# Kernel optimization log

Hardware: AMD Instinct MI355X
Metric: run time of the kernel (lower is better)

The kernel has to match this reference:

```python
import jax, jax.numpy as jnp
import numpy as np
from jax import lax

SCORE_THRESH = 0.05
NMS_THRESH = 0.5
DETECTIONS_PER_IMG = 100
MIN_SIZE = 0.01
AREA_THRESH = 0.0
BOX_W = (10.0, 10.0, 5.0, 5.0)
BBOX_XFORM_CLIP = float(np.log(1000.0 / 16.0))


def setup_inputs() -> dict:
    key = jax.random.key(0)
    B, N, C = 8, 4000, 91
    H, W = 800, 1333
    k1, k2, k3 = jax.random.split(key, 3)
    # scale logits so a realistic fraction of softmax scores exceed score_thresh
    class_logits = jax.random.normal(k1, (B * N, C), jnp.float32) * 2.0
    box_regression = jax.random.normal(k2, (B * N, C * 4), jnp.float32)
    u = jax.random.uniform(k3, (B, N, 4), jnp.float32)
    x1 = u[..., 0] * (W - 50)
    y1 = u[..., 1] * (H - 50)
    bw = u[..., 2] * 200.0 + 4.0
    bh = u[..., 3] * 200.0 + 4.0
    proposals = jnp.stack([x1, y1, jnp.minimum(x1 + bw, W), jnp.minimum(y1 + bh, H)], axis=-1)
    return {"class_logits": class_logits, "box_regression": box_regression,
            "proposals": proposals, "image_h": H, "image_w": W}


def _decode(rel, props):
    # torchvision BoxCoder.decode: props [P,4], rel [P, C*4] -> [P, C, 4]
    w = props[:, 2] - props[:, 0]
    h = props[:, 3] - props[:, 1]
    cx = props[:, 0] + 0.5 * w
    cy = props[:, 1] + 0.5 * h
    rel = rel.reshape(rel.shape[0], -1, 4)
    dx = rel[..., 0] / BOX_W[0]
    dy = rel[..., 1] / BOX_W[1]
    dw = jnp.minimum(rel[..., 2] / BOX_W[2], BBOX_XFORM_CLIP)
    dh = jnp.minimum(rel[..., 3] / BOX_W[3], BBOX_XFORM_CLIP)
    pcx = dx * w[:, None] + cx[:, None]
    pcy = dy * h[:, None] + cy[:, None]
    pw = jnp.exp(dw) * w[:, None]
    ph = jnp.exp(dh) * h[:, None]
    return jnp.stack([pcx - 0.5 * pw, pcy - 0.5 * ph, pcx + 0.5 * pw, pcy + 0.5 * ph], axis=-1)


def _nms_image(boxes, scores, labels_f, valid, off_unit):
    # greedy batched NMS (class-offset trick) producing first DETECTIONS_PER_IMG survivors
    NEG = -1e9
    s0 = jnp.where(valid, scores, NEG)
    ob = boxes + (labels_f * off_unit)[:, None]  # per-class coordinate offset
    areas = (ob[:, 2] - ob[:, 0]) * (ob[:, 3] - ob[:, 1])

    def step(s, _):
        i = jnp.argmax(s)
        sc = s[i]
        ok = sc > (NEG / 2)
        obi = ob[i]
        ix1 = jnp.maximum(obi[0], ob[:, 0])
        iy1 = jnp.maximum(obi[1], ob[:, 1])
        ix2 = jnp.minimum(obi[2], ob[:, 2])
        iy2 = jnp.minimum(obi[3], ob[:, 3])
        inter = jnp.maximum(ix2 - ix1, 0.0) * jnp.maximum(iy2 - iy1, 0.0)
        ai = (obi[2] - obi[0]) * (obi[3] - obi[1])
        iou = inter / jnp.maximum(ai + areas - inter, 1e-9)
        sup = (iou > NMS_THRESH) & ok
        s = jnp.where(sup, NEG, s).at[i].set(NEG)
        return s, (i, jnp.where(ok, sc, 0.0), ok)

    _, (idx, out_sc, ok) = lax.scan(step, s0, None, length=DETECTIONS_PER_IMG)
    out_boxes = boxes[idx] * ok[:, None]
    out_labels = jnp.where(ok, labels_f[idx], 0.0)
    areas_out = (out_boxes[:, 2] - out_boxes[:, 0]) * (out_boxes[:, 3] - out_boxes[:, 1])
    keep = ok & (areas_out >= AREA_THRESH)
    return out_boxes * keep[:, None], out_sc * keep, jnp.where(keep, out_labels, 0.0), keep


def reference(class_logits, box_regression, proposals, image_h, image_w):
    B, N, _ = proposals.shape
    C = class_logits.shape[-1]
    pred_boxes = _decode(box_regression, proposals.reshape(B * N, 4)).reshape(B, N, C, 4)
    pred_scores = jax.nn.softmax(class_logits, axis=-1).reshape(B, N, C)
    # clip boxes to image
    x = jnp.clip(pred_boxes[..., 0::2], 0.0, float(image_w))
    y = jnp.clip(pred_boxes[..., 1::2], 0.0, float(image_h))
    pred_boxes = jnp.stack([x[..., 0], y[..., 0], x[..., 1], y[..., 1]], axis=-1)
    # drop background class 0, flatten (proposal, class) pairs
    M = N * (C - 1)
    boxes = pred_boxes[:, :, 1:, :].reshape(B, M, 4)
    scores = pred_scores[:, :, 1:].reshape(B, M)
    labels_f = jnp.broadcast_to(jnp.arange(1, C, dtype=boxes.dtype)[None, :], (N, C - 1)).reshape(M)
    ws = boxes[..., 2] - boxes[..., 0]
    hs = boxes[..., 3] - boxes[..., 1]
    valid = (scores > SCORE_THRESH) & (ws >= MIN_SIZE) & (hs >= MIN_SIZE)
    off_unit = float(max(image_h, image_w)) + 1.0
    out_boxes, out_scores, out_labels_f, keep = jax.vmap(
        lambda b, s, v: _nms_image(b, s, labels_f, v, off_unit))(boxes, scores, valid)
    return out_boxes, out_scores, out_labels_f.astype(jnp.int32), keep
```

## Files before the change

### kernel.cpp

```cpp
#include <hip/hip_runtime.h>
#include <stdint.h>

typedef uint32_t u32;
typedef unsigned long long u64;

#define NB 8
#define NPER 4000
#define NC 91
#define NCLS 90
#define NDET 100
#define CHUNKS 64
#define RPB 63
#define LBIN 16
#define CCAP 63
#define BINCAP 512
#define SURVCAP 9216
#define NSFIX (NCLS * NDET)
#define FKCAP 1024
#define VPT 36

__device__ __forceinline__ float4 decode_clip(float4 rel, float w, float h,
                                              float cx, float cy, float W, float H) {
  const float XCLIP = 4.135166556742356f;
  float dx = rel.x / 10.0f;
  float dy = rel.y / 10.0f;
  float dw = fminf(rel.z / 5.0f, XCLIP);
  float dh = fminf(rel.w / 5.0f, XCLIP);
  float qcx = dx * w + cx;
  float qcy = dy * h + cy;
  float qw = expf(dw) * w;
  float qh = expf(dh) * h;
  float x1 = qcx - 0.5f * qw, y1 = qcy - 0.5f * qh;
  float x2 = qcx + 0.5f * qw, y2 = qcy + 0.5f * qh;
  x1 = fminf(fmaxf(x1, 0.0f), W);
  x2 = fminf(fmaxf(x2, 0.0f), W);
  y1 = fminf(fmaxf(y1, 0.0f), H);
  y2 = fminf(fmaxf(y2, 0.0f), H);
  return make_float4(x1, y1, x2, y2);
}

__device__ __forceinline__ float rdlane(float v, int sl) {
  return __int_as_float(__builtin_amdgcn_readlane(__float_as_int(v), sl));
}

__device__ __forceinline__ void emit_row(int r, int rl, int lane, float sA, float sB,
    float W, float H, const float4* __restrict__ props4, const float4* __restrict__ breg4,
    u32* s_cnt, u64 (*s_key)[LBIN], float4 (*s_box)[LBIN],
    size_t chbase, u64* __restrict__ bins_key, float4* __restrict__ bins_box) {
  bool eA_ok = (lane >= 1) && (sA > 0.05f);
  bool eB_ok = (lane < NC - 64) && (sB > 0.05f);
  if (!(eA_ok || eB_ok)) return;
  float4 p = props4[r];
  float w = p.z - p.x, h = p.w - p.y;
  float cx = p.x + 0.5f * w, cy = p.y + 0.5f * h;
  if (eA_ok) {
    float4 raw = decode_clip(breg4[(size_t)r * NC + lane], w, h, cx, cy, W, H);
    if (((raw.z - raw.x) >= 0.01f) && ((raw.w - raw.y) >= 0.01f)) {
      int ci = lane - 1;
      u32 orig = (u32)(rl * NCLS + ci);
      u64 key = ((u64)__float_as_uint(sA) << 22) | (u64)(0x3FFFFFu - orig);
      u32 lp = atomicAdd(&s_cnt[ci], 1u);
      if (lp < LBIN) { s_key[ci][lp] = key; s_box[ci][lp] = raw; }
      else if (lp < CCAP) {
        size_t o = (chbase + ci) * CCAP + lp;
        bins_key[o] = key; bins_box[o] = raw;
      }
    }
  }
  if (eB_ok) {
    float4 raw = decode_clip(breg4[(size_t)r * NC + 64 + lane], w, h, cx, cy, W, H);
    if (((raw.z - raw.x) >= 0.01f) && ((raw.w - raw.y) >= 0.01f)) {
      int ci = 63 + lane;
      u32 orig = (u32)(rl * NCLS + ci);
      u64 key = ((u64)__float_as_uint(sB) << 22) | (u64)(0x3FFFFFu - orig);
      u32 lp = atomicAdd(&s_cnt[ci], 1u);
      if (lp < LBIN) { s_key[ci][lp] = key; s_box[ci][lp] = raw; }
      else if (lp < CCAP) {
        size_t o = (chbase + ci) * CCAP + lp;
        bins_key[o] = key; bins_box[o] = raw;
      }
    }
  }
}

__global__ __launch_bounds__(1024) void k_score(const float* __restrict__ logits,
    const float* __restrict__ boxreg, const float* __restrict__ props,
    const int* __restrict__ dh, const int* __restrict__ dw,
    u32* cnt_g, u64* bins_key, float4* bins_box) {
  __shared__ u64 s_key[NCLS][LBIN];
  __shared__ float4 s_box[NCLS][LBIN];
  __shared__ u32 s_cnt[NCLS];
  int tid = threadIdx.x;
  int b = blockIdx.x / CHUNKS;
  int chunk = blockIdx.x % CHUNKS;
  int wave = tid >> 6, lane = tid & 63;
  if (tid < NCLS) s_cnt[tid] = 0u;
  __syncthreads();

  float H = (float)dh[0], W = (float)dw[0];
  const float4* props4 = (const float4*)props;
  const float4* breg4 = (const float4*)boxreg;
  size_t chbase = ((size_t)(b * CHUNKS + chunk)) * NCLS;

  for (int rloc = wave; rloc < RPB; rloc += 32) {
    int rloc1 = rloc + 16;
    int rl0 = chunk * RPB + rloc;
    int rl1 = chunk * RPB + rloc1;
    bool v0 = (rl0 < NPER);
    bool v1 = (rloc1 < RPB) && (rl1 < NPER);
    int r0 = b * NPER + (v0 ? rl0 : 0);
    int r1 = b * NPER + (v1 ? rl1 : 0);
    const float* l0 = logits + (size_t)r0 * NC;
    const float* l1 = logits + (size_t)r1 * NC;
    float xA0 = l0[lane];
    float xA1 = l1[lane];
    float xB0 = (lane < NC - 64) ? l0[64 + lane] : -3.0e38f;
    float xB1 = (lane < NC - 64) ? l1[64 + lane] : -3.0e38f;
    float mx0 = fmaxf(xA0, xB0);
    float mx1 = fmaxf(xA1, xB1);
    for (int o = 32; o; o >>= 1) {
      mx0 = fmaxf(mx0, __shfl_xor(mx0, o));
      mx1 = fmaxf(mx1, __shfl_xor(mx1, o));
    }
    float eA0 = expf(xA0 - mx0);
    float eA1 = expf(xA1 - mx1);
    float eB0 = (lane < NC - 64) ? expf(xB0 - mx0) : 0.0f;
    float eB1 = (lane < NC - 64) ? expf(xB1 - mx1) : 0.0f;
    float sm0 = eA0 + eB0;
    float sm1 = eA1 + eB1;
    for (int o = 32; o; o >>= 1) {
      sm0 += __shfl_xor(sm0, o);
      sm1 += __shfl_xor(sm1, o);
    }
    if (v0) emit_row(r0, rl0, lane, eA0 / sm0, eB0 / sm0, W, H, props4, breg4,
                     s_cnt, s_key, s_box, chbase, bins_key, bins_box);
    if (v1) emit_row(r1, rl1, lane, eA1 / sm1, eB1 / sm1, W, H, props4, breg4,
                     s_cnt, s_key, s_box, chbase, bins_key, bins_box);
  }
  __syncthreads();
  if (tid < NCLS) cnt_g[chbase + tid] = s_cnt[tid];
  for (int idx = tid; idx < NCLS * LBIN; idx += 1024) {
    int ci = idx / LBIN, j = idx % LBIN;
    if ((u32)j < s_cnt[ci]) {
      size_t o = (chbase + ci) * CCAP + (u32)j;
      bins_key[o] = s_key[ci][j];
      bins_box[o] = s_box[ci][j];
    }
  }
}

__global__ __launch_bounds__(256) void k_nms_class(const u32* __restrict__ cnt_g,
    const u64* __restrict__ bins_key, const float4* __restrict__ bins_box,
    u64* skey, float4* sbox, const int* __restrict__ dh, const int* __restrict__ dw) {
  __shared__ u64 k[BINCAP];
  __shared__ float4 boxu[BINCAP];
  __shared__ u64 ks[BINCAP];
  __shared__ float4 boxs[BINCAP];
  __shared__ float4 s_sb[NDET];
  __shared__ float s_sa[NDET];
  __shared__ u64 s_sk[NDET];
  __shared__ u32 s_sid[NDET];
  __shared__ u32 s_off[64];
  __shared__ u32 s_c[64];
  __shared__ u32 s_n;

  int b = blockIdx.x / NCLS;
  int ci = blockIdx.x % NCLS;
  int tid = threadIdx.x;
  u64* outk = skey + (size_t)b * SURVCAP + (size_t)ci * NDET;
  float4* outb = sbox + (size_t)b * SURVCAP + (size_t)ci * NDET;

  if (tid < 64) {
    u32 c = cnt_g[((size_t)(b * CHUNKS + tid)) * NCLS + ci];
    if (c > CCAP) c = CCAP;
    s_c[tid] = c;
    u32 inc = c;
    for (int o = 1; o < 64; o <<= 1) {
      u32 v = __shfl_up(inc, o);
      if (tid >= o) inc += v;
    }
    s_off[tid] = inc - c;
    if (tid == 63) s_n = (inc > BINCAP) ? BINCAP : inc;
  }
  __syncthreads();
  int n = (int)s_n;
  if (n <= 0) {
    for (int i = tid; i < NDET; i += 256) outk[i] = 0ull;
    return;
  }
  {
    int chunk = tid & 63, start = tid >> 6;
    u32 cc = s_c[chunk], of = s_off[chunk];
    size_t src = (((size_t)(b * CHUNKS + chunk)) * NCLS + ci) * CCAP;
    for (u32 i = (u32)start; i < cc; i += 4) {
      u32 d = of + i;
      if (d < (u32)BINCAP) { k[d] = bins_key[src + i]; boxu[d] = bins_box[src + i]; }
    }
  }
  __syncthreads();
  for (int i = tid; i < n; i += 256) {
    u64 ki = k[i];
    u32 rank = 0;
    int j = 0;
    for (; j + 4 <= n; j += 4) {
      rank += (k[j] > ki) ? 1u : 0u;
      rank += (k[j + 1] > ki) ? 1u : 0u;
      rank += (k[j + 2] > ki) ? 1u : 0u;
      rank += (k[j + 3] > ki) ? 1u : 0u;
    }
    for (; j < n; ++j) rank += (k[j] > ki) ? 1u : 0u;
    ks[rank] = ki;
    boxs[rank] = boxu[i];
  }
  __syncthreads();
  if (tid >= 64) return;

  float H = (float)dh[0], W = (float)dw[0];
  float loff = (fmaxf(H, W) + 1.0f) * (float)(ci + 1);
  int lane = tid;
  int S = 0;
  for (int base = 0; base < n && S < NDET; base += 64) {
    int i = base + lane;
    bool have = (i < n);
    u64 mykey = 0ull;
    float4 Bb = make_float4(0.f, 0.f, 0.f, 0.f);
    float aB = 0.f;
    if (have) {
      mykey = ks[i];
      float4 raw = boxs[i];
      Bb = make_float4(raw.x + loff, raw.y + loff, raw.z + loff, raw.w + loff);
      aB = (Bb.z - Bb.x) * (Bb.w - Bb.y);
    }
    bool alive = have;
    for (int s = 0; s < S; ++s) {
      float4 A = s_sb[s];
      float aA = s_sa[s];
      float ix1 = fmaxf(A.x, Bb.x), iy1 = fmaxf(A.y, Bb.y);
      float ix2 = fminf(A.z, Bb.z), iy2 = fminf(A.w, Bb.w);
      float inter = fmaxf(ix2 - ix1, 0.0f) * fmaxf(iy2 - iy1, 0.0f);
      float iou = inter / fmaxf(aA + aB - inter, 1e-9f);
      if (alive && iou > 0.5f) alive = false;
    }
    u64 mask = __ballot(alive);
    while (mask && S < NDET) {
      int j = __builtin_ctzll(mask);
      int js = __builtin_amdgcn_readfirstlane(j);
      float Ax = rdlane(Bb.x, js), Ay = rdlane(Bb.y, js);
      float Az = rdlane(Bb.z, js), Aw = rdlane(Bb.w, js);
      float aA = rdlane(aB, js);
      if (lane == js) {
        s_sb[S] = Bb; s_sa[S] = aB; s_sk[S] = mykey; s_sid[S] = (u32)i;
      }
      float ix1 = fmaxf(Ax, Bb.x), iy1 = fmaxf(Ay, Bb.y);
      float ix2 = fminf(Az, Bb.z), iy2 = fminf(Aw, Bb.w);
      float inter = fmaxf(ix2 - ix1, 0.0f) * fmaxf(iy2 - iy1, 0.0f);
      float iou = inter / fmaxf(aA + aB - inter, 1e-9f);
      if (alive && iou > 0.5f) alive = false;
      ++S;
      mask = __ballot(alive);
    }
  }
  for (int i2 = lane; i2 < NDET; i2 += 64) {
    if (i2 < S) {
      outk[i2] = s_sk[i2];
      outb[i2] = boxs[s_sid[i2]];
    } else {
      outk[i2] = 0ull;
    }
  }
}

__global__ __launch_bounds__(256) void k_top(const u64* __restrict__ skey,
    const float4* __restrict__ sbox, float* out) {
  __shared__ u32 ssc[SURVCAP];
  __shared__ u32 s_red[4];
  __shared__ u32 s_cnt[2];
  __shared__ u64 fk[FKCAP];
  __shared__ u32 fs[FKCAP];
  __shared__ u64 okey[NDET];
  __shared__ u32 osrc[NDET];

  int b = blockIdx.x;
  int tid = threadIdx.x;
  const u64* kb = skey + (size_t)b * SURVCAP;

  u32 sc[VPT];
#pragma unroll
  for (int v = 0; v < VPT; ++v) {
    u32 j = (u32)tid + (u32)v * 256u;
    u32 s = 0u;
    if (j < NSFIX) s = (u32)(kb[j] >> 22);
    sc[v] = s;
    ssc[j] = s;
  }
  if (tid == 0) { s_cnt[0] = 0; s_cnt[1] = 0; }
  __syncthreads();

  u32 lo = 0x3D4CCCCEu, hi = 0x3F800001u;
  while (lo < hi) {
    u32 mid = lo + ((hi - lo) >> 1);
    u32 c = 0;
#pragma unroll
    for (int v = 0; v < VPT; ++v) c += (sc[v] > mid) ? 1u : 0u;
    for (int o = 32; o; o >>= 1) c += __shfl_xor(c, o);
    if ((tid & 63) == 0) s_red[tid >> 6] = c;
    __syncthreads();
    u32 totc = s_red[0] + s_red[1] + s_red[2] + s_red[3];
    __syncthreads();
    if (totc < NDET) hi = mid; else lo = mid + 1;
  }
  u32 T = lo;
  __syncthreads();

  for (u32 j = tid; j < NSFIX; j += 256) {
    if (ssc[j] > T) {
      u32 p = atomicAdd(&s_cnt[0], 1u);
      if (p < FKCAP) { fk[p] = kb[j]; fs[p] = j; }
    }
  }
  __syncthreads();
  if (tid == 0) s_cnt[1] = s_cnt[0];
  __syncthreads();
  for (u32 j = tid; j < NSFIX; j += 256) {
    if (ssc[j] == T) {
      u32 p = atomicAdd(&s_cnt[1], 1u);
      if (p < FKCAP) { fk[p] = kb[j]; fs[p] = j; }
    }
  }
  __syncthreads();
  u32 tot = s_cnt[1];
  if (tot > FKCAP) tot = FKCAP;
  if (tid >= 64) return;

  for (int i = tid; i < NDET; i += 64) okey[i] = 0ull;
  for (int i = tid; i < (int)tot; i += 64) {
    u64 ki = fk[i];
    u32 rank = 0;
    for (int j = 0; j < (int)tot; ++j) rank += (fk[j] > ki) ? 1u : 0u;
    if (rank < NDET) { okey[rank] = ki; osrc[rank] = fs[i]; }
  }
  for (int i = tid; i < NDET; i += 64) {
    u64 key = okey[i];
    float b0 = 0.f, b1 = 0.f, b2 = 0.f, b3 = 0.f, sc2 = 0.f, lb = 0.f, kp = 0.f;
    if (key) {
      float4 bx = sbox[(size_t)b * SURVCAP + osrc[i]];
      b0 = bx.x; b1 = bx.y; b2 = bx.z; b3 = bx.w;
      sc2 = __uint_as_float((u32)(key >> 22));
      u32 orig = 0x3FFFFFu - (u32)(key & 0x3FFFFFu);
      lb = (float)(orig % NCLS + 1u);
      kp = 1.0f;
    }
    float* ob = out + ((size_t)b * NDET + i) * 4;
    ob[0] = b0; ob[1] = b1; ob[2] = b2; ob[3] = b3;
    out[NB * NDET * 4 + b * NDET + i] = sc2;
    out[NB * NDET * 5 + b * NDET + i] = lb;
    out[NB * NDET * 6 + b * NDET + i] = kp;
  }
}

extern "C" void kernel_launch(void* const* d_in, const int* in_sizes, int n_in,
                              void* d_out, int out_size, void* d_ws, size_t ws_size,
                              hipStream_t stream) {
  const float* logits = (const float*)d_in[0];
  const float* boxreg = (const float*)d_in[1];
  const float* props  = (const float*)d_in[2];
  const int* dh = (const int*)d_in[3];
  const int* dw = (const int*)d_in[4];
  float* out = (float*)d_out;

  char* ws = (char*)d_ws;
  u32* cnt_g = (u32*)ws;
  char* p0 = ws + (((size_t)NB * CHUNKS * NCLS * 4 + 255) & ~(size_t)255);
  u64* bins_key = (u64*)p0;
  char* p1 = p0 + (size_t)NB * CHUNKS * NCLS * CCAP * 8;
  float4* bins_box = (float4*)p1;
  char* p2 = p1 + (size_t)NB * CHUNKS * NCLS * CCAP * 16;
  u64* skey = (u64*)p2;
  float4* sbox = (float4*)(p2 + (size_t)NB * SURVCAP * 8);
  (void)ws_size;

  k_score<<<NB * CHUNKS, 1024, 0, stream>>>(logits, boxreg, props, dh, dw,
                                            cnt_g, bins_key, bins_box);
  k_nms_class<<<NB * NCLS, 256, 0, stream>>>(cnt_g, bins_key, bins_box,
                                             skey, sbox, dh, dw);
  k_top<<<NB, 256, 0, stream>>>(skey, sbox, out);
}
```

Baseline: 172.2 us.

## Fuse per-class NMS and top-k kernels via last-block-done atomic counter

Merges the per-class NMS kernel and the per-image top-100 selection kernel into one launch. Each class block bumps a per-image atomic counter after writing its survivors, and the last block to finish runs the top-k merge. This removes one kernel launch and its inter-kernel gap. The top-k pass also reads candidate scores from registers instead of a large shared-memory score array, which shrinks the fused kernel's LDS footprint. The cost is that the final merge runs on whichever block finishes last, and correctness depends on the fences and on the counter being reset in the first kernel.

```diff
diff --git a/kernel.cpp b/kernel.cpp
--- a/kernel.cpp
+++ b/kernel.cpp
@@ -86,7 +86,7 @@
 __global__ __launch_bounds__(1024) void k_score(const float* __restrict__ logits,
     const float* __restrict__ boxreg, const float* __restrict__ props,
     const int* __restrict__ dh, const int* __restrict__ dw,
-    u32* cnt_g, u64* bins_key, float4* bins_box) {
+    u32* cnt_g, u64* bins_key, float4* bins_box, u32* done) {
   __shared__ u64 s_key[NCLS][LBIN];
   __shared__ float4 s_box[NCLS][LBIN];
   __shared__ u32 s_cnt[NCLS];
@@ -94,6 +94,8 @@
   int b = blockIdx.x / CHUNKS;
   int chunk = blockIdx.x % CHUNKS;
   int wave = tid >> 6, lane = tid & 63;
+  if (tid == 0 && chunk == 0)
+    __hip_atomic_store(&done[b], 0u, __ATOMIC_RELAXED, __HIP_MEMORY_SCOPE_AGENT);
   if (tid < NCLS) s_cnt[tid] = 0u;
   __syncthreads();
 
@@ -149,20 +151,24 @@
   }
 }
 
-__global__ __launch_bounds__(256) void k_nms_class(const u32* __restrict__ cnt_g,
+__global__ __launch_bounds__(256) void k_nms_top(const u32* __restrict__ cnt_g,
     const u64* __restrict__ bins_key, const float4* __restrict__ bins_box,
-    u64* skey, float4* sbox, const int* __restrict__ dh, const int* __restrict__ dw) {
-  __shared__ u64 k[BINCAP];
-  __shared__ float4 boxu[BINCAP];
-  __shared__ u64 ks[BINCAP];
-  __shared__ float4 boxs[BINCAP];
-  __shared__ float4 s_sb[NDET];
-  __shared__ float s_sa[NDET];
-  __shared__ u64 s_sk[NDET];
-  __shared__ u32 s_sid[NDET];
-  __shared__ u32 s_off[64];
-  __shared__ u32 s_c[64];
-  __shared__ u32 s_n;
+    u64* __restrict__ skey, float4* __restrict__ sbox,
+    const int* __restrict__ dh, const int* __restrict__ dw,
+    u32* done, float* __restrict__ out) {
+  __shared__ __align__(16) char sm[28352];
+  u64* kk = (u64*)sm;
+  float4* boxu = (float4*)(sm + 4096);
+  u64* ks = (u64*)(sm + 12288);
+  float4* boxs = (float4*)(sm + 16384);
+  float4* s_sb = (float4*)(sm + 24576);
+  float* s_sa = (float*)(sm + 26176);
+  u64* s_sk = (u64*)(sm + 26576);
+  u32* s_sid = (u32*)(sm + 27376);
+  u32* s_off = (u32*)(sm + 27776);
+  u32* s_c = (u32*)(sm + 28032);
+  u32* s_n = (u32*)(sm + 28288);
+  u32* s_last = (u32*)(sm + 28292);
 
   int b = blockIdx.x / NCLS;
   int ci = blockIdx.x % NCLS;
@@ -180,120 +186,122 @@
       if (tid >= o) inc += v;
     }
     s_off[tid] = inc - c;
-    if (tid == 63) s_n = (inc > BINCAP) ? BINCAP : inc;
-  }
-  __syncthreads();
-  int n = (int)s_n;
-  if (n <= 0) {
+    if (tid == 63) *s_n = (inc > BINCAP) ? BINCAP : inc;
+  }
+  __syncthreads();
+  int n = (int)*s_n;
+  if (n > 0) {
+    {
+      int chunk = tid & 63, start = tid >> 6;
+      u32 cc = s_c[chunk], of = s_off[chunk];
+      size_t src = (((size_t)(b * CHUNKS + chunk)) * NCLS + ci) * CCAP;
+      for (u32 i = (u32)start; i < cc; i += 4) {
+        u32 d = of + i;
+        if (d < (u32)BINCAP) { kk[d] = bins_key[src + i]; boxu[d] = bins_box[src + i]; }
+      }
+    }
+    __syncthreads();
+    for (int i = tid; i < n; i += 256) {
+      u64 ki = kk[i];
+      u32 rank = 0;
+      int j = 0;
+      for (; j + 4 <= n; j += 4) {
+        rank += (kk[j] > ki) ? 1u : 0u;
+        rank += (kk[j + 1] > ki) ? 1u : 0u;
+        rank += (kk[j + 2] > ki) ? 1u : 0u;
+        rank += (kk[j + 3] > ki) ? 1u : 0u;
+      }
+      for (; j < n; ++j) rank += (kk[j] > ki) ? 1u : 0u;
+      ks[rank] = ki;
+      boxs[rank] = boxu[i];
+    }
+    __syncthreads();
+    if (tid < 64) {
+      float H = (float)dh[0], W = (float)dw[0];
+      float loff = (fmaxf(H, W) + 1.0f) * (float)(ci + 1);
+      int lane = tid;
+      int S = 0;
+      for (int base = 0; base < n && S < NDET; base += 64) {
+        int i = base + lane;
+        bool have = (i < n);
+        u64 mykey = 0ull;
+        float4 Bb = make_float4(0.f, 0.f, 0.f, 0.f);
+        float aB = 0.f;
+        if (have) {
+          mykey = ks[i];
+          float4 raw = boxs[i];
+          Bb = make_float4(raw.x + loff, raw.y + loff, raw.z + loff, raw.w + loff);
+          aB = (Bb.z - Bb.x) * (Bb.w - Bb.y);
+        }
+        bool alive = have;
+        for (int s = 0; s < S; ++s) {
+          float4 A = s_sb[s];
+          float aA = s_sa[s];
+          float ix1 = fmaxf(A.x, Bb.x), iy1 = fmaxf(A.y, Bb.y);
+          float ix2 = fminf(A.z, Bb.z), iy2 = fminf(A.w, Bb.w);
+          float inter = fmaxf(ix2 - ix1, 0.0f) * fmaxf(iy2 - iy1, 0.0f);
+          float iou = inter / fmaxf(aA + aB - inter, 1e-9f);
+          if (alive && iou > 0.5f) alive = false;
+        }
+        u64 mask = __ballot(alive);
+        while (mask && S < NDET) {
+          int j = __builtin_ctzll(mask);
+          int js = __builtin_amdgcn_readfirstlane(j);
+          float Ax = rdlane(Bb.x, js), Ay = rdlane(Bb.y, js);
+          float Az = rdlane(Bb.z, js), Aw = rdlane(Bb.w, js);
+          float aA = rdlane(aB, js);
+          if (lane == js) {
+            s_sb[S] = Bb; s_sa[S] = aB; s_sk[S] = mykey; s_sid[S] = (u32)i;
+          }
+          float ix1 = fmaxf(Ax, Bb.x), iy1 = fmaxf(Ay, Bb.y);
+          float ix2 = fminf(Az, Bb.z), iy2 = fminf(Aw, Bb.w);
+          float inter = fmaxf(ix2 - ix1, 0.0f) * fmaxf(iy2 - iy1, 0.0f);
+          float iou = inter / fmaxf(aA + aB - inter, 1e-9f);
+          if (alive && iou > 0.5f) alive = false;
+          ++S;
+          mask = __ballot(alive);
+        }
+      }
+      for (int i2 = lane; i2 < NDET; i2 += 64) {
+        if (i2 < S) {
+          outk[i2] = s_sk[i2];
+          outb[i2] = boxs[s_sid[i2]];
+        } else {
+          outk[i2] = 0ull;
+        }
+      }
+    }
+  } else {
     for (int i = tid; i < NDET; i += 256) outk[i] = 0ull;
-    return;
-  }
-  {
-    int chunk = tid & 63, start = tid >> 6;
-    u32 cc = s_c[chunk], of = s_off[chunk];
-    size_t src = (((size_t)(b * CHUNKS + chunk)) * NCLS + ci) * CCAP;
-    for (u32 i = (u32)start; i < cc; i += 4) {
-      u32 d = of + i;
-      if (d < (u32)BINCAP) { k[d] = bins_key[src + i]; boxu[d] = bins_box[src + i]; }
-    }
-  }
-  __syncthreads();
-  for (int i = tid; i < n; i += 256) {
-    u64 ki = k[i];
-    u32 rank = 0;
-    int j = 0;
-    for (; j + 4 <= n; j += 4) {
-      rank += (k[j] > ki) ? 1u : 0u;
-      rank += (k[j + 1] > ki) ? 1u : 0u;
-      rank += (k[j + 2] > ki) ? 1u : 0u;
-      rank += (k[j + 3] > ki) ? 1u : 0u;
-    }
-    for (; j < n; ++j) rank += (k[j] > ki) ? 1u : 0u;
-    ks[rank] = ki;
-    boxs[rank] = boxu[i];
-  }
-  __syncthreads();
-  if (tid >= 64) return;
-
-  float H = (float)dh[0], W = (float)dw[0];
-  float loff = (fmaxf(H, W) + 1.0f) * (float)(ci + 1);
-  int lane = tid;
-  int S = 0;
-  for (int base = 0; base < n && S < NDET; base += 64) {
-    int i = base + lane;
-    bool have = (i < n);
-    u64 mykey = 0ull;
-    float4 Bb = make_float4(0.f, 0.f, 0.f, 0.f);
-    float aB = 0.f;
-    if (have) {
-      mykey = ks[i];
-      float4 raw = boxs[i];
-      Bb = make_float4(raw.x + loff, raw.y + loff, raw.z + loff, raw.w + loff);
-      aB = (Bb.z - Bb.x) * (Bb.w - Bb.y);
-    }
-    bool alive = have;
-    for (int s = 0; s < S; ++s) {
-      float4 A = s_sb[s];
-      float aA = s_sa[s];
-      float ix1 = fmaxf(A.x, Bb.x), iy1 = fmaxf(A.y, Bb.y);
-      float ix2 = fminf(A.z, Bb.z), iy2 = fminf(A.w, Bb.w);
-      float inter = fmaxf(ix2 - ix1, 0.0f) * fmaxf(iy2 - iy1, 0.0f);
-      float iou = inter / fmaxf(aA + aB - inter, 1e-9f);
-      if (alive && iou > 0.5f) alive = false;
-    }
-    u64 mask = __ballot(alive);
-    while (mask && S < NDET) {
-      int j = __builtin_ctzll(mask);
-      int js = __builtin_amdgcn_readfirstlane(j);
-      float Ax = rdlane(Bb.x, js), Ay = rdlane(Bb.y, js);
-      float Az = rdlane(Bb.z, js), Aw = rdlane(Bb.w, js);
-      float aA = rdlane(aB, js);
-      if (lane == js) {
-        s_sb[S] = Bb; s_sa[S] = aB; s_sk[S] = mykey; s_sid[S] = (u32)i;
-      }
-      float ix1 = fmaxf(Ax, Bb.x), iy1 = fmaxf(Ay, Bb.y);
-      float ix2 = fminf(Az, Bb.z), iy2 = fminf(Aw, Bb.w);
-      float inter = fmaxf(ix2 - ix1, 0.0f) * fmaxf(iy2 - iy1, 0.0f);
-      float iou = inter / fmaxf(aA + aB - inter, 1e-9f);
-      if (alive && iou > 0.5f) alive = false;
-      ++S;
-      mask = __ballot(alive);
-    }
-  }
-  for (int i2 = lane; i2 < NDET; i2 += 64) {
-    if (i2 < S) {
-      outk[i2] = s_sk[i2];
-      outb[i2] = boxs[s_sid[i2]];
-    } else {
-      outk[i2] = 0ull;
-    }
-  }
-}
-
-__global__ __launch_bounds__(256) void k_top(const u64* __restrict__ skey,
-    const float4* __restrict__ sbox, float* out) {
-  __shared__ u32 ssc[SURVCAP];
-  __shared__ u32 s_red[4];
-  __shared__ u32 s_cnt[2];
-  __shared__ u64 fk[FKCAP];
-  __shared__ u32 fs[FKCAP];
-  __shared__ u64 okey[NDET];
-  __shared__ u32 osrc[NDET];
-
-  int b = blockIdx.x;
-  int tid = threadIdx.x;
+  }
+
+  __syncthreads();
+  if (tid == 0) {
+    __threadfence();
+    u32 old = __hip_atomic_fetch_add(&done[b], 1u, __ATOMIC_ACQ_REL,
+                                     __HIP_MEMORY_SCOPE_AGENT);
+    u32 last = (old == (u32)(NCLS - 1)) ? 1u : 0u;
+    if (last) __threadfence();
+    *s_last = last;
+  }
+  __syncthreads();
+  if (!*s_last) return;
+
   const u64* kb = skey + (size_t)b * SURVCAP;
+  u64* fk = (u64*)sm;
+  u32* fs = (u32*)(sm + 8192);
+  u64* okey = (u64*)(sm + 12288);
+  u32* osrc = (u32*)(sm + 13088);
+  u32* s_red = (u32*)(sm + 13488);
+  u32* s_cnt2 = (u32*)(sm + 13504);
 
   u32 sc[VPT];
 #pragma unroll
   for (int v = 0; v < VPT; ++v) {
     u32 j = (u32)tid + (u32)v * 256u;
-    u32 s = 0u;
-    if (j < NSFIX) s = (u32)(kb[j] >> 22);
-    sc[v] = s;
-    ssc[j] = s;
-  }
-  if (tid == 0) { s_cnt[0] = 0; s_cnt[1] = 0; }
+    sc[v] = (j < NSFIX) ? (u32)(kb[j] >> 22) : 0u;
+  }
+  if (tid == 0) { s_cnt2[0] = 0; s_cnt2[1] = 0; }
   __syncthreads();
 
   u32 lo = 0x3D4CCCCEu, hi = 0x3F800001u;
@@ -312,23 +320,27 @@
   u32 T = lo;
   __syncthreads();
 
-  for (u32 j = tid; j < NSFIX; j += 256) {
-    if (ssc[j] > T) {
-      u32 p = atomicAdd(&s_cnt[0], 1u);
+#pragma unroll
+  for (int v = 0; v < VPT; ++v) {
+    u32 j = (u32)tid + (u32)v * 256u;
+    if (j < NSFIX && sc[v] > T) {
+      u32 p = atomicAdd(&s_cnt2[0], 1u);
       if (p < FKCAP) { fk[p] = kb[j]; fs[p] = j; }
     }
   }
   __syncthreads();
-  if (tid == 0) s_cnt[1] = s_cnt[0];
-  __syncthreads();
-  for (u32 j = tid; j < NSFIX; j += 256) {
-    if (ssc[j] == T) {
-      u32 p = atomicAdd(&s_cnt[1], 1u);
+  if (tid == 0) s_cnt2[1] = s_cnt2[0];
+  __syncthreads();
+#pragma unroll
+  for (int v = 0; v < VPT; ++v) {
+    u32 j = (u32)tid + (u32)v * 256u;
+    if (j < NSFIX && sc[v] == T) {
+      u32 p = atomicAdd(&s_cnt2[1], 1u);
       if (p < FKCAP) { fk[p] = kb[j]; fs[p] = j; }
     }
   }
   __syncthreads();
-  u32 tot = s_cnt[1];
+  u32 tot = s_cnt2[1];
   if (tot > FKCAP) tot = FKCAP;
   if (tid >= 64) return;
 
@@ -377,11 +389,11 @@
   char* p2 = p1 + (size_t)NB * CHUNKS * NCLS * CCAP * 16;
   u64* skey = (u64*)p2;
   float4* sbox = (float4*)(p2 + (size_t)NB * SURVCAP * 8);
+  u32* done = (u32*)(p2 + (size_t)NB * SURVCAP * 8 + (size_t)NB * SURVCAP * 16);
   (void)ws_size;
 
   k_score<<<NB * CHUNKS, 1024, 0, stream>>>(logits, boxreg, props, dh, dw,
-                                            cnt_g, bins_key, bins_box);
-  k_nms_class<<<NB * NCLS, 256, 0, stream>>>(cnt_g, bins_key, bins_box,
-                                             skey, sbox, dh, dw);
-  k_top<<<NB, 256, 0, stream>>>(skey, sbox, out);
-}
+                                            cnt_g, bins_key, bins_box, done);
+  k_nms_top<<<NB * NCLS, 256, 0, stream>>>(cnt_g, bins_key, bins_box,
+                                           skey, sbox, dh, dw, done, out);
+}
```

After: 192.9 us. 12.0% more time.

## Replace bisection threshold search in top-k with shared-memory histogram bin selection

Applied to the files above, without the earlier changes.

The final top-100 selection kernel previously binary-searched the score threshold with about 30 block-wide count-and-reduce rounds, each needing two barriers. It now builds one shared-memory histogram over score bits, finds the cutoff bin with a single-wave suffix scan, and gathers candidates above and inside that bin straight from registers. This removes the large score array in shared memory and most barriers. In exchange, a dense cutoff bin could push candidates past FKCAP and silently drop some.

```diff
diff --git a/kernel.cpp b/kernel.cpp
--- a/kernel.cpp
+++ b/kernel.cpp
@@ -18,6 +18,9 @@
 #define NSFIX (NCLS * NDET)
 #define FKCAP 1024
 #define VPT 36
+#define NBIN 1152
+#define SLO 0x3D4CCCCEu
+#define SSH 15
 
 __device__ __forceinline__ float4 decode_clip(float4 rel, float w, float h,
                                               float cx, float cy, float W, float H) {
@@ -272,13 +275,13 @@
 
 __global__ __launch_bounds__(256) void k_top(const u64* __restrict__ skey,
     const float4* __restrict__ sbox, float* out) {
-  __shared__ u32 ssc[SURVCAP];
-  __shared__ u32 s_red[4];
-  __shared__ u32 s_cnt[2];
+  __shared__ u32 hist[NBIN];
   __shared__ u64 fk[FKCAP];
   __shared__ u32 fs[FKCAP];
   __shared__ u64 okey[NDET];
   __shared__ u32 osrc[NDET];
+  __shared__ u32 s_cnt[2];
+  __shared__ u32 s_bin;
 
   int b = blockIdx.x;
   int tid = threadIdx.x;
@@ -288,32 +291,52 @@
 #pragma unroll
   for (int v = 0; v < VPT; ++v) {
     u32 j = (u32)tid + (u32)v * 256u;
-    u32 s = 0u;
-    if (j < NSFIX) s = (u32)(kb[j] >> 22);
-    sc[v] = s;
-    ssc[j] = s;
-  }
+    sc[v] = (j < NSFIX) ? (u32)(kb[j] >> 22) : 0u;
+  }
+  for (int i = tid; i < NBIN; i += 256) hist[i] = 0u;
   if (tid == 0) { s_cnt[0] = 0; s_cnt[1] = 0; }
   __syncthreads();
 
-  u32 lo = 0x3D4CCCCEu, hi = 0x3F800001u;
-  while (lo < hi) {
-    u32 mid = lo + ((hi - lo) >> 1);
-    u32 c = 0;
 #pragma unroll
-    for (int v = 0; v < VPT; ++v) c += (sc[v] > mid) ? 1u : 0u;
-    for (int o = 32; o; o >>= 1) c += __shfl_xor(c, o);
-    if ((tid & 63) == 0) s_red[tid >> 6] = c;
-    __syncthreads();
-    u32 totc = s_red[0] + s_red[1] + s_red[2] + s_red[3];
-    __syncthreads();
-    if (totc < NDET) hi = mid; else lo = mid + 1;
-  }
-  u32 T = lo;
-  __syncthreads();
-
-  for (u32 j = tid; j < NSFIX; j += 256) {
-    if (ssc[j] > T) {
+  for (int v = 0; v < VPT; ++v) {
+    u32 s = sc[v];
+    if (s > SLO) atomicAdd(&hist[(s - SLO) >> SSH], 1u);
+  }
+  __syncthreads();
+
+  if (tid < 64) {
+    int lane = tid;
+    int base = lane * (NBIN / 64);
+    u32 csum = 0;
+#pragma unroll
+    for (int kk2 = 0; kk2 < NBIN / 64; ++kk2) csum += hist[base + kk2];
+    u32 suf = csum;
+    for (int o = 1; o < 64; o <<= 1) {
+      u32 v = __shfl_down(suf, o);
+      if (lane + o < 64) suf += v;
+    }
+    u64 m = __ballot(suf >= NDET);
+    int B = 0;
+    if (m) {
+      int c = 63 - __builtin_clzll(m);
+      u32 rest = (c < 63) ? (u32)__shfl((int)suf, c + 1) : 0u;
+      u32 acc = rest;
+      int cb = c * (NBIN / 64);
+      for (int kk2 = (NBIN / 64) - 1; kk2 >= 0; --kk2) {
+        acc += hist[cb + kk2];
+        if (acc >= NDET) { B = cb + kk2; break; }
+      }
+    }
+    if (lane == 0) s_bin = (u32)B;
+  }
+  __syncthreads();
+  u32 B = s_bin;
+
+#pragma unroll
+  for (int v = 0; v < VPT; ++v) {
+    u32 s = sc[v];
+    if (s > SLO && ((s - SLO) >> SSH) > B) {
+      u32 j = (u32)tid + (u32)v * 256u;
       u32 p = atomicAdd(&s_cnt[0], 1u);
       if (p < FKCAP) { fk[p] = kb[j]; fs[p] = j; }
     }
@@ -321,8 +344,11 @@
   __syncthreads();
   if (tid == 0) s_cnt[1] = s_cnt[0];
   __syncthreads();
-  for (u32 j = tid; j < NSFIX; j += 256) {
-    if (ssc[j] == T) {
+#pragma unroll
+  for (int v = 0; v < VPT; ++v) {
+    u32 s = sc[v];
+    if (s > SLO && ((s - SLO) >> SSH) == B) {
+      u32 j = (u32)tid + (u32)v * 256u;
       u32 p = atomicAdd(&s_cnt[1], 1u);
       if (p < FKCAP) { fk[p] = kb[j]; fs[p] = j; }
     }
```

After: 159.2 us. 1.08x faster.
